# Optimization experiments

Measured on AMD Instinct MI355X. Metric: run time of the kernel, lower is better.

The kernel has to match this reference:

```python
import jax, jax.numpy as jnp
import numpy as np

N_HEADS = 4
D_K = 64
SCALE = D_K ** (-0.5)


def setup_inputs() -> dict:
    key = jax.random.key(0)
    k1, k2, k3, k4, k5 = jax.random.split(key, 5)
    B, C, H, W = 16, 256, 32, 32
    x = jax.random.normal(k1, (B, C, H, W), dtype=jnp.float32)
    # Linear weights stored as (in, out) for x @ W convention
    w_qkv = jax.random.normal(k2, (C, N_HEADS * D_K * 3), dtype=jnp.float32) * (C ** -0.5)
    b_qkv = jax.random.normal(k3, (N_HEADS * D_K * 3,), dtype=jnp.float32) * 0.02
    w_out = jax.random.normal(k4, (N_HEADS * D_K, C), dtype=jnp.float32) * ((N_HEADS * D_K) ** -0.5)
    b_out = jax.random.normal(k5, (C,), dtype=jnp.float32) * 0.02
    return {"x": x, "w_qkv": w_qkv, "b_qkv": b_qkv, "w_out": w_out, "b_out": b_out}


def reference(x, w_qkv, b_qkv, w_out, b_out):
    # NOTE: the original torch module defines GroupNorm but never applies it
    # in forward; we faithfully reproduce the forward as written.
    B, C, H, W = x.shape
    S = H * W
    xs = x.reshape(B, C, S).transpose(0, 2, 1)            # [B, S, C]
    qkv = (xs @ w_qkv + b_qkv).reshape(B, S, N_HEADS, 3 * D_K)
    q, k, v = jnp.split(qkv, 3, axis=-1)                   # each [B, S, H, d_k]
    attn = jnp.einsum('bihd,bjhd->bijh', q, k) * SCALE     # [B, S, S, H]
    attn = jax.nn.softmax(attn, axis=2)                    # softmax over j (keys)
    res = jnp.einsum('bijh,bjhd->bihd', attn, v)           # [B, S, H, d_k]
    res = res.reshape(B, S, N_HEADS * D_K)
    res = res @ w_out + b_out + xs                         # residual add
    return res.transpose(0, 2, 1).reshape(B, C, H, W)
```

## Files before the change

### kernel.cpp

```cpp
#include <hip/hip_runtime.h>
#include <hip/hip_bf16.h>

typedef __attribute__((ext_vector_type(8))) short short8;
typedef __attribute__((ext_vector_type(4))) short short4v;
typedef __attribute__((ext_vector_type(4))) float floatx4;
typedef unsigned short u16;

#define SCL_LOG2E 0.1803368801111204f

__device__ inline u16 f2b(float f) {
  __hip_bfloat16 h = __float2bfloat16(f);
  union { __hip_bfloat16 h; u16 u; } cv; cv.h = h; return cv.u;
}

__global__ __launch_bounds__(256) void wprep(const float* __restrict__ w1,
                                             const float* __restrict__ w2,
                                             u16* __restrict__ o1,
                                             u16* __restrict__ o2) {
  __shared__ u16 tile[64][72];
  const int R = 256;
  const float* in; u16* out; int Cc, cb;
  if (blockIdx.x < 12) { in = w1; out = o1; Cc = 768; cb = blockIdx.x; }
  else                 { in = w2; out = o2; Cc = 256; cb = blockIdx.x - 12; }
  int c0 = cb * 64, r0 = blockIdx.y * 64;
  int tx = threadIdx.x, ty = threadIdx.y;
#pragma unroll
  for (int i = 0; i < 4; i++) {
    int r = ty + 16 * i;
    float4 v = *(const float4*)&in[(size_t)(r0 + r) * Cc + c0 + tx * 4];
    tile[tx * 4 + 0][r] = f2b(v.x);
    tile[tx * 4 + 1][r] = f2b(v.y);
    tile[tx * 4 + 2][r] = f2b(v.z);
    tile[tx * 4 + 3][r] = f2b(v.w);
  }
  __syncthreads();
#pragma unroll
  for (int i = 0; i < 4; i++) {
    int cc = ty + 16 * i;
    ushort4 o = *(ushort4*)&tile[cc][tx * 4];
    *(ushort4*)&out[(size_t)(c0 + cc) * R + r0 + tx * 4] = o;
  }
}

__global__ __launch_bounds__(256, 3) void qkv_gemm(const float* __restrict__ x,
                                                   const u16* __restrict__ wT,
                                                   const float* __restrict__ bias,
                                                   u16* __restrict__ Qo,
                                                   u16* __restrict__ Ko,
                                                   u16* __restrict__ Vto) {
  __shared__ u16 As[2][128 * 36];
  const int tid = threadIdx.x, wave = tid >> 6, lane = tid & 63;
  const int l15 = lane & 15, quad = lane >> 4;
  const int wm = (wave >> 1) * 64, wn = (wave & 1) * 64;
  const int m0 = blockIdx.x * 128, n0 = blockIdx.y * 128;
  const int bb = m0 >> 10, s0 = m0 & 1023;
  const int cr = tid >> 3, uu = tid & 7;

  const float* xrow = x + ((size_t)bb * 256 + cr) * 1024 + s0 + uu * 4;
  const u16* wrow[4];
#pragma unroll
  for (int ni = 0; ni < 4; ni++)
    wrow[ni] = wT + (size_t)(n0 + wn + ni * 16 + l15) * 256 + quad * 8;

  floatx4 acc[4][4] = {};
  float4 LA[4];
  short8 bfr[4], nbf[4];

#pragma unroll
  for (int r = 0; r < 4; r++) LA[r] = *(const float4*)&xrow[r * 32];
#pragma unroll
  for (int ni = 0; ni < 4; ni++) bfr[ni] = *(const short8*)&wrow[ni][0];
#pragma unroll
  for (int r = 0; r < 4; r++) {
    int s = uu * 4 + r * 32;
    As[0][(s + 0) * 36 + cr] = f2b(LA[r].x);
    As[0][(s + 1) * 36 + cr] = f2b(LA[r].y);
    As[0][(s + 2) * 36 + cr] = f2b(LA[r].z);
    As[0][(s + 3) * 36 + cr] = f2b(LA[r].w);
  }

  int cur = 0;
  for (int kt8 = 0; kt8 < 8; kt8++) {
    const int kt = kt8 * 32;
    if (kt8 < 7) {
#pragma unroll
      for (int r = 0; r < 4; r++)
        LA[r] = *(const float4*)&xrow[(size_t)(kt + 32) * 1024 + r * 32];
#pragma unroll
      for (int ni = 0; ni < 4; ni++)
        nbf[ni] = *(const short8*)&wrow[ni][kt + 32];
    }
    __syncthreads();
    short8 af[4];
#pragma unroll
    for (int mi = 0; mi < 4; mi++) {
      const u16* p = &As[cur][(wm + mi * 16 + l15) * 36 + quad * 8];
      ushort4 lo = *(const ushort4*)p;
      ushort4 hi = *(const ushort4*)(p + 4);
      short8 v;
      v[0] = lo.x; v[1] = lo.y; v[2] = lo.z; v[3] = lo.w;
      v[4] = hi.x; v[5] = hi.y; v[6] = hi.z; v[7] = hi.w;
      af[mi] = v;
    }
#pragma unroll
    for (int mi = 0; mi < 4; mi++)
#pragma unroll
      for (int ni = 0; ni < 4; ni++)
        acc[mi][ni] = __builtin_amdgcn_mfma_f32_16x16x32_bf16(af[mi], bfr[ni],
                                                              acc[mi][ni], 0, 0, 0);
    __syncthreads();
    if (kt8 < 7) {
      u16* d = &As[cur ^ 1][0];
#pragma unroll
      for (int r = 0; r < 4; r++) {
        int s = uu * 4 + r * 32;
        d[(s + 0) * 36 + cr] = f2b(LA[r].x);
        d[(s + 1) * 36 + cr] = f2b(LA[r].y);
        d[(s + 2) * 36 + cr] = f2b(LA[r].z);
        d[(s + 3) * 36 + cr] = f2b(LA[r].w);
      }
#pragma unroll
      for (int ni = 0; ni < 4; ni++) bfr[ni] = nbf[ni];
      cur ^= 1;
    }
  }

#pragma unroll
  for (int ni = 0; ni < 4; ni++) {
    int n = n0 + wn + ni * 16 + l15;
    float bvv = bias[n];
    int h = n / 192;
    int rem = n - h * 192;
#pragma unroll
    for (int mi = 0; mi < 4; mi++) {
      int gm = m0 + wm + mi * 16 + quad * 4;
      int s = gm & 1023;
      if (rem < 128) {
        u16* dst;
        float scl;
        if (rem < 64) { dst = Qo; scl = SCL_LOG2E; } else { dst = Ko; scl = 1.0f; }
        int d = rem & 63;
#pragma unroll
        for (int r = 0; r < 4; r++)
          dst[((size_t)(bb * 4 + h) * 1024 + s + r) * 64 + d] =
              f2b((acc[mi][ni][r] + bvv) * scl);
      } else {
        int d = rem - 128;
        ushort4 pk;
        pk.x = f2b(acc[mi][ni][0] + bvv);
        pk.y = f2b(acc[mi][ni][1] + bvv);
        pk.z = f2b(acc[mi][ni][2] + bvv);
        pk.w = f2b(acc[mi][ni][3] + bvv);
        *(ushort4*)&Vto[((size_t)(bb * 4 + h) * 64 + d) * 1024 + s] = pk;
      }
    }
  }
}

__global__ __launch_bounds__(256, 2) void attn_kern(const u16* __restrict__ Q,
                                                    const u16* __restrict__ K,
                                                    const u16* __restrict__ Vt,
                                                    u16* __restrict__ O) {
  __shared__ u16 kv[3 * 2 * 64 * 72];
  const int bh = blockIdx.x;
  const u16* Qp = Q + (size_t)bh * 64 * 1024;
  const u16* Kp = K + (size_t)bh * 64 * 1024;
  const u16* Vp = Vt + (size_t)bh * 64 * 1024;
  u16* Op = O + (size_t)bh * 64 * 1024;
  const int q0 = blockIdx.y * 128;
  const int tid = threadIdx.x, wave = tid >> 6, lane = tid & 63;
  const int l15 = lane & 15, quad = lane >> 4;

  short8 qa[2][2];
#pragma unroll
  for (int qi = 0; qi < 2; qi++)
#pragma unroll
    for (int kh = 0; kh < 2; kh++)
      qa[qi][kh] = *(const short8*)&Qp[(size_t)(q0 + wave * 32 + qi * 16 + l15) * 64 +
                                       kh * 32 + quad * 8];

  const int srow = tid >> 2;
  const int sc = (tid & 3) * 16;
  const size_t kRow = (size_t)srow * 64 + sc;
  const size_t vRow = (size_t)srow * 1024 + sc;

  short8 t0k0 = *(const short8*)&Kp[kRow];
  short8 t0k1 = *(const short8*)&Kp[kRow + 8];
  short8 t0v0 = *(const short8*)&Vp[vRow];
  short8 t0v1 = *(const short8*)&Vp[vRow + 8];
  short8 t1k0 = *(const short8*)&Kp[kRow + 4096];
  short8 t1k1 = *(const short8*)&Kp[kRow + 4096 + 8];
  short8 t1v0 = *(const short8*)&Vp[vRow + 64];
  short8 t1v1 = *(const short8*)&Vp[vRow + 64 + 8];
  short8 r1k0 = *(const short8*)&Kp[kRow + 8192];
  short8 r1k1 = *(const short8*)&Kp[kRow + 8192 + 8];
  short8 r1v0 = *(const short8*)&Vp[vRow + 128];
  short8 r1v1 = *(const short8*)&Vp[vRow + 128 + 8];
  *(short8*)&kv[srow * 72 + sc] = t0k0;
  *(short8*)&kv[srow * 72 + sc + 8] = t0k1;
  *(short8*)&kv[4608 + srow * 72 + sc] = t0v0;
  *(short8*)&kv[4608 + srow * 72 + sc + 8] = t0v1;
  *(short8*)&kv[9216 + srow * 72 + sc] = t1k0;
  *(short8*)&kv[9216 + srow * 72 + sc + 8] = t1k1;
  *(short8*)&kv[9216 + 4608 + srow * 72 + sc] = t1v0;
  *(short8*)&kv[9216 + 4608 + srow * 72 + sc + 8] = t1v1;
  __syncthreads();

  float lsum[2] = {0.f, 0.f};
  floatx4 acc[2][4] = {};

  int cur = 0;
  int wr = 2;
  for (int t = 0; t < 16; t++) {
    const u16* Ksb = kv + cur * 9216;
    const u16* Vsb = Ksb + 4608;

    short8 r2k0, r2k1, r2v0, r2v1;
    if (t < 13) {
      size_t ko = kRow + (size_t)(t + 3) * 4096;
      size_t vo = vRow + (size_t)(t + 3) * 64;
      r2k0 = *(const short8*)&Kp[ko];
      r2k1 = *(const short8*)&Kp[ko + 8];
      r2v0 = *(const short8*)&Vp[vo];
      r2v1 = *(const short8*)&Vp[vo + 8];
    }

    short8 kb[4][2];
#pragma unroll
    for (int mj = 0; mj < 4; mj++)
#pragma unroll
      for (int kh = 0; kh < 2; kh++)
        kb[mj][kh] = *(const short8*)&Ksb[(mj * 16 + l15) * 72 + kh * 32 + quad * 8];

    floatx4 sf[2][4];
#pragma unroll
    for (int qi = 0; qi < 2; qi++)
#pragma unroll
      for (int mj = 0; mj < 4; mj++) {
        floatx4 z = {};
        z = __builtin_amdgcn_mfma_f32_16x16x32_bf16(kb[mj][0], qa[qi][0], z, 0, 0, 0);
        sf[qi][mj] =
            __builtin_amdgcn_mfma_f32_16x16x32_bf16(kb[mj][1], qa[qi][1], z, 0, 0, 0);
      }

    short4v pb[2][4];
#pragma unroll
    for (int qi = 0; qi < 2; qi++)
#pragma unroll
      for (int mj = 0; mj < 4; mj++) {
        float p0 = exp2f(sf[qi][mj][0]), p1 = exp2f(sf[qi][mj][1]);
        float p2 = exp2f(sf[qi][mj][2]), p3 = exp2f(sf[qi][mj][3]);
        lsum[qi] += (p0 + p1) + (p2 + p3);
        short4v pk;
        pk[0] = (short)f2b(p0); pk[1] = (short)f2b(p1);
        pk[2] = (short)f2b(p2); pk[3] = (short)f2b(p3);
        pb[qi][mj] = pk;
      }

#pragma unroll
    for (int c = 0; c < 4; c++)
#pragma unroll
      for (int md = 0; md < 4; md++) {
        short4v va = *(const short4v*)&Vsb[(md * 16 + l15) * 72 + c * 16 + quad * 4];
#pragma unroll
        for (int qi = 0; qi < 2; qi++)
          acc[qi][md] =
              __builtin_amdgcn_mfma_f32_16x16x16bf16_1k(va, pb[qi][c], acc[qi][md],
                                                        0, 0, 0);
      }

    if (t < 14) {
      u16* dst = kv + wr * 9216;
      *(short8*)&dst[srow * 72 + sc] = r1k0;
      *(short8*)&dst[srow * 72 + sc + 8] = r1k1;
      *(short8*)&dst[4608 + srow * 72 + sc] = r1v0;
      *(short8*)&dst[4608 + srow * 72 + sc + 8] = r1v1;
    }
    r1k0 = r2k0; r1k1 = r2k1; r1v0 = r2v0; r1v1 = r2v1;
    cur = (cur == 2) ? 0 : cur + 1;
    wr = (wr == 2) ? 0 : wr + 1;
    __syncthreads();
  }

  float inv[2];
#pragma unroll
  for (int qi = 0; qi < 2; qi++) {
    lsum[qi] += __shfl_xor(lsum[qi], 16, 64);
    lsum[qi] += __shfl_xor(lsum[qi], 32, 64);
    inv[qi] = 1.f / lsum[qi];
  }

  u16* Ot = kv;
#pragma unroll
  for (int qi = 0; qi < 2; qi++)
#pragma unroll
    for (int md = 0; md < 4; md++) {
      uint2 pk;
      u16 a0 = f2b(acc[qi][md][0] * inv[qi]), a1 = f2b(acc[qi][md][1] * inv[qi]);
      u16 a2 = f2b(acc[qi][md][2] * inv[qi]), a3 = f2b(acc[qi][md][3] * inv[qi]);
      pk.x = (unsigned)a0 | ((unsigned)a1 << 16);
      pk.y = (unsigned)a2 | ((unsigned)a3 << 16);
      *(uint2*)&Ot[(wave * 32 + qi * 16 + l15) * 72 + md * 16 + quad * 4] = pk;
    }
  __syncthreads();
#pragma unroll
  for (int rr = 0; rr < 4; rr++) {
    int row = wave * 32 + (lane >> 3) + 8 * rr;
    int col = (lane & 7) * 8;
    short8 v = *(const short8*)&Ot[row * 72 + col];
    *(short8*)&Op[(size_t)(q0 + row) * 64 + col] = v;
  }
}

__global__ __launch_bounds__(256) void out_gemm(const u16* __restrict__ Oin,
                                                const u16* __restrict__ wT,
                                                const float* __restrict__ bias,
                                                const float* __restrict__ x,
                                                float* __restrict__ out) {
  __shared__ u16 As[64 * 32];
  const int tid = threadIdx.x, wave = tid >> 6, lane = tid & 63;
  const int l15 = lane & 15, quad = lane >> 4;
  const int wm = (wave >> 1) * 32, wn = (wave & 1) * 64;
  const int m0 = blockIdx.x * 64, n0 = blockIdx.y * 128;
  const int bb = m0 >> 10, s0 = m0 & 1023;
  const int ar = tid >> 2, ach = (tid & 3) * 8;

  const u16* wrow[4];
#pragma unroll
  for (int ni = 0; ni < 4; ni++)
    wrow[ni] = wT + (size_t)(n0 + wn + ni * 16 + l15) * 256 + quad * 8;

  floatx4 acc[2][4] = {};
  short8 LA, bfr[4], nbf[4];

  LA = *(const short8*)&Oin[((size_t)(bb * 4) * 1024 + s0 + ar) * 64 + ach];
#pragma unroll
  for (int ni = 0; ni < 4; ni++) bfr[ni] = *(const short8*)&wrow[ni][0];
  *(short8*)&As[ar * 32 + ach] = LA;

  for (int kt8 = 0; kt8 < 8; kt8++) {
    const int kt = kt8 * 32;
    if (kt8 < 7) {
      int kn = kt + 32, h = kn >> 6, d0 = kn & 63;
      LA = *(const short8*)&Oin[((size_t)(bb * 4 + h) * 1024 + s0 + ar) * 64 + d0 + ach];
#pragma unroll
      for (int ni = 0; ni < 4; ni++) nbf[ni] = *(const short8*)&wrow[ni][kn];
    }
    __syncthreads();
    short8 af[2];
#pragma unroll
    for (int mi = 0; mi < 2; mi++)
      af[mi] = *(short8*)&As[(wm + mi * 16 + l15) * 32 + quad * 8];
#pragma unroll
    for (int mi = 0; mi < 2; mi++)
#pragma unroll
      for (int ni = 0; ni < 4; ni++)
        acc[mi][ni] = __builtin_amdgcn_mfma_f32_16x16x32_bf16(af[mi], bfr[ni],
                                                              acc[mi][ni], 0, 0, 0);
    __syncthreads();
    if (kt8 < 7) {
      *(short8*)&As[ar * 32 + ach] = LA;
#pragma unroll
      for (int ni = 0; ni < 4; ni++) bfr[ni] = nbf[ni];
    }
  }

#pragma unroll
  for (int ni = 0; ni < 4; ni++) {
    int c = n0 + wn + ni * 16 + l15;
    float bvv = bias[c];
#pragma unroll
    for (int mi = 0; mi < 2; mi++) {
      int gm = m0 + wm + mi * 16 + quad * 4;
      int s = gm & 1023;
      size_t idx = ((size_t)bb * 256 + c) * 1024 + s;
      float4 xr = *(const float4*)&x[idx];
      float4 o;
      o.x = acc[mi][ni][0] + bvv + xr.x;
      o.y = acc[mi][ni][1] + bvv + xr.y;
      o.z = acc[mi][ni][2] + bvv + xr.z;
      o.w = acc[mi][ni][3] + bvv + xr.w;
      *(float4*)&out[idx] = o;
    }
  }
}

extern "C" void kernel_launch(void* const* d_in, const int* in_sizes, int n_in,
                              void* d_out, int out_size, void* d_ws, size_t ws_size,
                              hipStream_t stream) {
  const float* x     = (const float*)d_in[0];
  const float* w_qkv = (const float*)d_in[1];
  const float* b_qkv = (const float*)d_in[2];
  const float* w_out = (const float*)d_in[3];
  const float* b_out = (const float*)d_in[4];
  float* out = (float*)d_out;
  char* ws = (char*)d_ws;

  u16* wT1 = (u16*)(ws);
  u16* wT2 = (u16*)(ws + 0x80000);
  u16* Qb  = (u16*)(ws + 0x100000);
  u16* Kb  = (u16*)(ws + 0x900000);
  u16* Vtb = (u16*)(ws + 0x1100000);
  u16* Ob  = (u16*)(ws + 0x1900000);

  wprep<<<dim3(16, 4), dim3(16, 16), 0, stream>>>(w_qkv, w_out, wT1, wT2);
  qkv_gemm<<<dim3(128, 6), 256, 0, stream>>>(x, wT1, b_qkv, Qb, Kb, Vtb);
  attn_kern<<<dim3(64, 8), 256, 0, stream>>>(Qb, Kb, Vtb, Ob);
  out_gemm<<<dim3(256, 2), 256, 0, stream>>>(Ob, wT2, b_out, x, out);
}
```

Before: 140.0 us.

## Switch attention K/V pipeline to double buffering with higher occupancy and MFMA priority

Replaces the triple-buffered LDS ring with register prefetch two tiles ahead by a two-buffer scheme that prefetches only one tile ahead. This cuts LDS per block from about 55KB to about 37KB and register pressure, so launch bounds rise to 3 blocks per CU. It also wraps the MFMA sections in s_setprio to favour matrix issue across waves. The cost is shallower prefetch, which gives less time to hide global-load latency in each iteration.

```diff
diff --git a/kernel.cpp b/kernel.cpp
--- a/kernel.cpp
+++ b/kernel.cpp
@@ -157,11 +157,11 @@
   }
 }
 
-__global__ __launch_bounds__(256, 2) void attn_kern(const u16* __restrict__ Q,
+__global__ __launch_bounds__(256, 3) void attn_kern(const u16* __restrict__ Q,
                                                     const u16* __restrict__ K,
                                                     const u16* __restrict__ Vt,
                                                     u16* __restrict__ O) {
-  __shared__ u16 kv[3 * 2 * 64 * 72];
+  __shared__ u16 kv[2 * 2 * 64 * 72];
   const int bh = blockIdx.x;
   const u16* Qp = Q + (size_t)bh * 64 * 1024;
   const u16* Kp = K + (size_t)bh * 64 * 1024;
@@ -183,46 +183,36 @@
   const int sc = (tid & 3) * 16;
   const size_t kRow = (size_t)srow * 64 + sc;
   const size_t vRow = (size_t)srow * 1024 + sc;
-
-  short8 t0k0 = *(const short8*)&Kp[kRow];
-  short8 t0k1 = *(const short8*)&Kp[kRow + 8];
-  short8 t0v0 = *(const short8*)&Vp[vRow];
-  short8 t0v1 = *(const short8*)&Vp[vRow + 8];
-  short8 t1k0 = *(const short8*)&Kp[kRow + 4096];
-  short8 t1k1 = *(const short8*)&Kp[kRow + 4096 + 8];
-  short8 t1v0 = *(const short8*)&Vp[vRow + 64];
-  short8 t1v1 = *(const short8*)&Vp[vRow + 64 + 8];
-  short8 r1k0 = *(const short8*)&Kp[kRow + 8192];
-  short8 r1k1 = *(const short8*)&Kp[kRow + 8192 + 8];
-  short8 r1v0 = *(const short8*)&Vp[vRow + 128];
-  short8 r1v1 = *(const short8*)&Vp[vRow + 128 + 8];
-  *(short8*)&kv[srow * 72 + sc] = t0k0;
-  *(short8*)&kv[srow * 72 + sc + 8] = t0k1;
-  *(short8*)&kv[4608 + srow * 72 + sc] = t0v0;
-  *(short8*)&kv[4608 + srow * 72 + sc + 8] = t0v1;
-  *(short8*)&kv[9216 + srow * 72 + sc] = t1k0;
-  *(short8*)&kv[9216 + srow * 72 + sc + 8] = t1k1;
-  *(short8*)&kv[9216 + 4608 + srow * 72 + sc] = t1v0;
-  *(short8*)&kv[9216 + 4608 + srow * 72 + sc + 8] = t1v1;
+  const int lk0 = srow * 72 + sc;
+  const int lv0 = 4608 + srow * 72 + sc;
+
+  {
+    short8 t0k0 = *(const short8*)&Kp[kRow];
+    short8 t0k1 = *(const short8*)&Kp[kRow + 8];
+    short8 t0v0 = *(const short8*)&Vp[vRow];
+    short8 t0v1 = *(const short8*)&Vp[vRow + 8];
+    *(short8*)&kv[lk0] = t0k0;
+    *(short8*)&kv[lk0 + 8] = t0k1;
+    *(short8*)&kv[lv0] = t0v0;
+    *(short8*)&kv[lv0 + 8] = t0v1;
+  }
   __syncthreads();
 
   float lsum[2] = {0.f, 0.f};
   floatx4 acc[2][4] = {};
 
-  int cur = 0;
-  int wr = 2;
   for (int t = 0; t < 16; t++) {
-    const u16* Ksb = kv + cur * 9216;
+    const u16* Ksb = kv + (t & 1) * 9216;
     const u16* Vsb = Ksb + 4608;
 
-    short8 r2k0, r2k1, r2v0, r2v1;
-    if (t < 13) {
-      size_t ko = kRow + (size_t)(t + 3) * 4096;
-      size_t vo = vRow + (size_t)(t + 3) * 64;
-      r2k0 = *(const short8*)&Kp[ko];
-      r2k1 = *(const short8*)&Kp[ko + 8];
-      r2v0 = *(const short8*)&Vp[vo];
-      r2v1 = *(const short8*)&Vp[vo + 8];
+    short8 rk0, rk1, rv0, rv1;
+    if (t < 15) {
+      size_t ko = kRow + (size_t)(t + 1) * 4096;
+      size_t vo = vRow + (size_t)(t + 1) * 64;
+      rk0 = *(const short8*)&Kp[ko];
+      rk1 = *(const short8*)&Kp[ko + 8];
+      rv0 = *(const short8*)&Vp[vo];
+      rv1 = *(const short8*)&Vp[vo + 8];
     }
 
     short8 kb[4][2];
@@ -233,6 +223,7 @@
         kb[mj][kh] = *(const short8*)&Ksb[(mj * 16 + l15) * 72 + kh * 32 + quad * 8];
 
     floatx4 sf[2][4];
+    __builtin_amdgcn_s_setprio(1);
 #pragma unroll
     for (int qi = 0; qi < 2; qi++)
 #pragma unroll
@@ -242,6 +233,7 @@
         sf[qi][mj] =
             __builtin_amdgcn_mfma_f32_16x16x32_bf16(kb[mj][1], qa[qi][1], z, 0, 0, 0);
       }
+    __builtin_amdgcn_s_setprio(0);
 
     short4v pb[2][4];
 #pragma unroll
@@ -257,6 +249,7 @@
         pb[qi][mj] = pk;
       }
 
+    __builtin_amdgcn_s_setprio(1);
 #pragma unroll
     for (int c = 0; c < 4; c++)
 #pragma unroll
@@ -268,17 +261,15 @@
               __builtin_amdgcn_mfma_f32_16x16x16bf16_1k(va, pb[qi][c], acc[qi][md],
                                                         0, 0, 0);
       }
-
-    if (t < 14) {
-      u16* dst = kv + wr * 9216;
-      *(short8*)&dst[srow * 72 + sc] = r1k0;
-      *(short8*)&dst[srow * 72 + sc + 8] = r1k1;
-      *(short8*)&dst[4608 + srow * 72 + sc] = r1v0;
-      *(short8*)&dst[4608 + srow * 72 + sc + 8] = r1v1;
-    }
-    r1k0 = r2k0; r1k1 = r2k1; r1v0 = r2v0; r1v1 = r2v1;
-    cur = (cur == 2) ? 0 : cur + 1;
-    wr = (wr == 2) ? 0 : wr + 1;
+    __builtin_amdgcn_s_setprio(0);
+
+    if (t < 15) {
+      u16* dst = kv + ((t + 1) & 1) * 9216;
+      *(short8*)&dst[lk0] = rk0;
+      *(short8*)&dst[lk0 + 8] = rk1;
+      *(short8*)&dst[lv0] = rv0;
+      *(short8*)&dst[lv0 + 8] = rv1;
+    }
     __syncthreads();
   }
 
```

New measurement: 142.6 us. About the same (+1.9%).
